# Performance work log

Hardware: AMD Instinct MI355X
Metric: run time of the kernel (lower is better)

The kernel has to match this reference:

```python
import jax, jax.numpy as jnp
import numpy as np

D_MODEL = 1024
D_STATE = 16
D_CONV = 4
EXPAND = 2
D_INNER = D_MODEL * EXPAND


def setup_inputs() -> dict:
    key = jax.random.key(0)
    ks = jax.random.split(key, 10)
    B, L = 2, 2048
    x = jax.random.normal(ks[0], (B, L, D_MODEL), jnp.float32)
    W_in = jax.random.normal(ks[1], (2 * D_INNER, D_MODEL), jnp.float32) * (1.0 / np.sqrt(D_MODEL))
    conv_w = jax.random.normal(ks[2], (D_INNER, 1, D_CONV), jnp.float32) * (1.0 / np.sqrt(D_CONV))
    conv_b = jax.random.normal(ks[3], (D_INNER,), jnp.float32) * 0.1
    W_x = jax.random.normal(ks[4], (2 * D_STATE + 1, D_INNER), jnp.float32) * (1.0 / np.sqrt(D_INNER))
    A_log = jnp.log(jnp.abs(jax.random.normal(ks[5], (D_INNER, D_STATE), jnp.float32)) + 1e-4)
    D_param = jnp.ones((D_INNER,), jnp.float32)
    W_dt = jax.random.normal(ks[6], (D_INNER, 1), jnp.float32)
    b_dt = jax.random.normal(ks[7], (D_INNER,), jnp.float32) * 0.1
    W_out = jax.random.normal(ks[8], (D_MODEL, D_INNER), jnp.float32) * (1.0 / np.sqrt(D_INNER))
    return {"x": x, "W_in": W_in, "conv_w": conv_w, "conv_b": conv_b, "W_x": W_x,
            "A_log": A_log, "D_param": D_param, "W_dt": W_dt, "b_dt": b_dt, "W_out": W_out}


def _forward(x, W_in, conv_w, conv_b, W_x, A_log, D_param, W_dt, b_dt, W_out):
    B, L, _ = x.shape
    xz = x @ W_in.T                                  # [B,L,2*d_inner]
    x_ssm, z = jnp.split(xz, 2, axis=-1)
    # causal depthwise conv: torch pads both sides d_conv-1 then truncates to L == left-pad only
    xc = jnp.transpose(x_ssm, (0, 2, 1))             # [B,d_inner,L]
    xc = jax.lax.conv_general_dilated(
        xc, conv_w, window_strides=(1,), padding=[(D_CONV - 1, 0)],
        feature_group_count=D_INNER, dimension_numbers=("NCH", "OIH", "NCH"))
    xc = xc + conv_b[None, :, None]
    x_ssm = jax.nn.silu(jnp.transpose(xc, (0, 2, 1)))  # [B,L,d_inner]
    proj = x_ssm @ W_x.T                              # [B,L,2*d_state+1]
    B_ssm = proj[..., :D_STATE]                       # [B,L,d_state]
    C_ssm = proj[..., D_STATE:2 * D_STATE]            # [B,L,d_state]
    dt = jax.nn.softplus(proj[..., -1:] * W_dt[:, 0] + b_dt)  # [B,L,d_inner]
    A = -jnp.exp(A_log)                               # [d_inner,d_state]

    def step(h, inp):
        dt_t, Bt, Ct, xt = inp                        # [B,d_inner],[B,n],[B,n],[B,d_inner]
        dA = jnp.exp(dt_t[..., None] * A)             # [B,d_inner,d_state]
        h = dA * h + (xt * dt_t)[..., None] * Bt[:, None, :]
        y = jnp.einsum("bdn,bn->bd", h, Ct)
        return h, y

    h0 = jnp.zeros((B, D_INNER, D_STATE), x.dtype)
    inputs = (jnp.transpose(dt, (1, 0, 2)), jnp.transpose(B_ssm, (1, 0, 2)),
              jnp.transpose(C_ssm, (1, 0, 2)), jnp.transpose(x_ssm, (1, 0, 2)))
    _, ys = jax.lax.scan(step, h0, inputs)            # ys: [L,B,d_inner]
    y = jnp.transpose(ys, (1, 0, 2)) + x_ssm * D_param
    y = y * jax.nn.silu(z)
    return y @ W_out.T


def reference(x, W_in, conv_w, conv_b, W_x, A_log, D_param, W_dt, b_dt, W_out):
    return _forward(x, W_in, conv_w, conv_b, W_x, A_log, D_param, W_dt, b_dt, W_out)
```

## Files before the change

### kernel.cpp

```cpp
#include <hip/hip_runtime.h>
#include <hip/hip_bf16.h>
#include <cstddef>

#define DMODEL 1024
#define DI     2048
#define DS     16
#define LSEQ   2048
#define BATCH  2
#define NC     128
#define TCH    (LSEQ / NC)

typedef __attribute__((ext_vector_type(8))) short short8;
typedef __attribute__((ext_vector_type(4))) float f32x4;
typedef __attribute__((ext_vector_type(2))) float f32x2;
typedef __attribute__((ext_vector_type(8))) unsigned short us8;

__device__ __forceinline__ unsigned short f2bf(float f) {
    unsigned int u = __float_as_uint(f);
    unsigned int r = (u + 0x7fff + ((u >> 16) & 1)) >> 16;
    return (unsigned short)r;
}
__device__ __forceinline__ float bf2f(unsigned short b) {
    return __uint_as_float(((unsigned int)b) << 16);
}

__device__ __forceinline__ float fexp2(float x) {
#if __has_builtin(__builtin_amdgcn_exp2f)
    return __builtin_amdgcn_exp2f(x);
#else
    return exp2f(x);
#endif
}
__device__ __forceinline__ float flog2(float x) {
#if __has_builtin(__builtin_amdgcn_logf)
    return __builtin_amdgcn_logf(x);
#else
    return log2f(x);
#endif
}

#define LOG2E 1.4426950408889634f
#define RLOG2E 0.6931471805599453f

__device__ __forceinline__ float softplus_f(float v) {
    return (v > 20.f) ? v : flog2(1.f + fexp2(v * LOG2E)) * RLOG2E;
}

__device__ __forceinline__ void gload_lds16(const void* g, void* l) {
    __builtin_amdgcn_global_load_lds(
        (const __attribute__((address_space(1))) unsigned int*)g,
        (__attribute__((address_space(3))) unsigned int*)l, 16, 0, 0);
}

__global__ void cvt_bf16(const float* __restrict__ in, unsigned short* __restrict__ out, int n8) {
    int i = blockIdx.x * 256 + threadIdx.x;
    if (i >= n8) return;
    const float4* p = reinterpret_cast<const float4*>(in) + i * 2;
    float4 v0 = p[0], v1 = p[1];
    us8 o;
    o[0] = f2bf(v0.x); o[1] = f2bf(v0.y); o[2] = f2bf(v0.z); o[3] = f2bf(v0.w);
    o[4] = f2bf(v1.x); o[5] = f2bf(v1.y); o[6] = f2bf(v1.z); o[7] = f2bf(v1.w);
    *reinterpret_cast<us8*>(out + (size_t)i * 8) = o;
}

__global__ void prep_wx(const float* __restrict__ wx, unsigned short* __restrict__ out) {
    int i = blockIdx.x * 256 + threadIdx.x;
    if (i >= 48 * 2048 / 8) return;
    size_t o = (size_t)i * 8;
    int row = (int)(o >> 11);
    us8 v;
    if (row < 33) {
        const float4* p = reinterpret_cast<const float4*>(wx + o);
        float4 v0 = p[0], v1 = p[1];
        v[0] = f2bf(v0.x); v[1] = f2bf(v0.y); v[2] = f2bf(v0.z); v[3] = f2bf(v0.w);
        v[4] = f2bf(v1.x); v[5] = f2bf(v1.y); v[6] = f2bf(v1.z); v[7] = f2bf(v1.w);
    } else {
        v = (us8)0;
    }
    *reinterpret_cast<us8*>(out + o) = v;
}

__global__ void prep_A(const float* __restrict__ A_log, float* __restrict__ At2) {
    int i = blockIdx.x * 256 + threadIdx.x;
    if (i >= DS * DI) return;
    int n = i / DI, d = i % DI;
    At2[i] = -__expf(A_log[d * DS + n]) * LOG2E;
}

#define NT1 32
__global__ __launch_bounds__(512, 1)
void gemm1_pipe(const unsigned short* __restrict__ A, const unsigned short* __restrict__ B,
                unsigned short* __restrict__ C) {
    __shared__ unsigned short lds[4][2][256 * 32];

    const int tid = threadIdx.x;
    const int wid = tid >> 6, ln = tid & 63;
    const int wm = wid >> 2, wn = wid & 3;

    int wg = blockIdx.x;
    wg = (wg & 7) * 32 + (wg >> 3);
    const int m0 = (wg >> 4) * 256;
    const int n0 = (wg & 15) * 256;

    const int srow = tid >> 2;
    const int sun  = tid & 3;
    const int ksrc = ((sun ^ ((srow >> 1) & 3)) * 8);

    const int fr = ln & 15;
    const int fku = (ln >> 4);

    f32x4 acc[8][4] = {};

    #define STAGE1(kt)                                                                     \
        do {                                                                               \
            const int bq_ = (kt) & 3;                                                      \
            gload_lds16(A + (size_t)(m0 + srow) * 1024 + (kt) * 32 + ksrc,                 \
                        &lds[bq_][0][srow * 32 + sun * 8]);                                \
            gload_lds16(A + (size_t)(m0 + 128 + srow) * 1024 + (kt) * 32 + ksrc,           \
                        &lds[bq_][0][(128 + srow) * 32 + sun * 8]);                        \
            gload_lds16(B + (size_t)(n0 + srow) * 1024 + (kt) * 32 + ksrc,                 \
                        &lds[bq_][1][srow * 32 + sun * 8]);                                \
            gload_lds16(B + (size_t)(n0 + 128 + srow) * 1024 + (kt) * 32 + ksrc,           \
                        &lds[bq_][1][(128 + srow) * 32 + sun * 8]);                        \
        } while (0)

    STAGE1(0); STAGE1(1); STAGE1(2);
    asm volatile("s_waitcnt vmcnt(8)" ::: "memory");
    __builtin_amdgcn_s_barrier();
    __builtin_amdgcn_sched_barrier(0);

    for (int kt = 0; kt < NT1; ++kt) {
        const int bq = kt & 3;
        if (kt + 3 < NT1) STAGE1(kt + 3);

        short8 af_lo[4], bfr[4], af_hi[4];
        #pragma unroll
        for (int i = 0; i < 4; ++i) {
            int r = wm * 128 + i * 16 + fr;
            int u = fku ^ ((r >> 1) & 3);
            af_lo[i] = *reinterpret_cast<const short8*>(&lds[bq][0][r * 32 + u * 8]);
        }
        #pragma unroll
        for (int j = 0; j < 4; ++j) {
            int r = wn * 64 + j * 16 + fr;
            int u = fku ^ ((r >> 1) & 3);
            bfr[j] = *reinterpret_cast<const short8*>(&lds[bq][1][r * 32 + u * 8]);
        }
        #pragma unroll
        for (int i = 0; i < 4; ++i) {
            int r = wm * 128 + (4 + i) * 16 + fr;
            int u = fku ^ ((r >> 1) & 3);
            af_hi[i] = *reinterpret_cast<const short8*>(&lds[bq][0][r * 32 + u * 8]);
        }
        __builtin_amdgcn_sched_barrier(0);
        __builtin_amdgcn_s_setprio(1);
        #pragma unroll
        for (int i = 0; i < 4; ++i)
            #pragma unroll
            for (int j = 0; j < 4; ++j)
                acc[i][j] = __builtin_amdgcn_mfma_f32_16x16x32_bf16(af_lo[i], bfr[j], acc[i][j], 0, 0, 0);
        __builtin_amdgcn_s_setprio(0);
        __builtin_amdgcn_sched_barrier(0);
        __builtin_amdgcn_s_setprio(1);
        #pragma unroll
        for (int i = 0; i < 4; ++i)
            #pragma unroll
            for (int j = 0; j < 4; ++j)
                acc[4 + i][j] = __builtin_amdgcn_mfma_f32_16x16x32_bf16(af_hi[i], bfr[j], acc[4 + i][j], 0, 0, 0);
        __builtin_amdgcn_s_setprio(0);
        __builtin_amdgcn_sched_barrier(0);

        if (kt < NT1 - 3)       asm volatile("s_waitcnt vmcnt(8)" ::: "memory");
        else if (kt == NT1 - 3) asm volatile("s_waitcnt vmcnt(4)" ::: "memory");
        else if (kt == NT1 - 2) asm volatile("s_waitcnt vmcnt(0)" ::: "memory");
        __builtin_amdgcn_s_barrier();
        __builtin_amdgcn_sched_barrier(0);
    }
    #undef STAGE1

    const int cr = (ln >> 4) * 4, cc = ln & 15;
    #pragma unroll
    for (int i = 0; i < 8; ++i) {
        int row = m0 + wm * 128 + i * 16 + cr;
        #pragma unroll
        for (int j = 0; j < 4; ++j) {
            int col = n0 + wn * 64 + j * 16 + cc;
            #pragma unroll
            for (int r = 0; r < 4; ++r)
                C[(size_t)(row + r) * 4096 + col] = f2bf(acc[i][j][r]);
        }
    }
}

#define NT3 64
__global__ __launch_bounds__(256, 2)
void gemm3_pipe(const unsigned short* __restrict__ A, int lda,
                const unsigned short* __restrict__ B,
                float* __restrict__ C) {
    __shared__ unsigned short As[4][128 * 32];
    __shared__ unsigned short Bs[4][64 * 32];

    const int tid = threadIdx.x;
    const int wid = tid >> 6, ln = tid & 63;
    const int wm = wid >> 1, wn = wid & 1;

    int wg = blockIdx.x;
    wg = (wg & 7) * 64 + (wg >> 3);
    const int m0 = (wg >> 4) * 128;
    const int n0 = (wg & 15) * 64;

    const int srow = tid >> 2;
    const int sun  = tid & 3;
    const int ksrc = ((sun ^ ((srow >> 1) & 3)) * 8);

    const int fr = ln & 15;
    const int fku = (ln >> 4);

    f32x4 acc[4][2] = {};

    #define STAGE3(kt)                                                                     \
        do {                                                                               \
            const int bq_ = (kt) & 3;                                                      \
            gload_lds16(A + (size_t)(m0 + srow) * lda + (kt) * 32 + ksrc,                  \
                        &As[bq_][srow * 32 + sun * 8]);                                    \
            gload_lds16(A + (size_t)(m0 + 64 + srow) * lda + (kt) * 32 + ksrc,             \
                        &As[bq_][(64 + srow) * 32 + sun * 8]);                             \
            gload_lds16(B + (size_t)(n0 + srow) * 2048 + (kt) * 32 + ksrc,                 \
                        &Bs[bq_][srow * 32 + sun * 8]);                                    \
        } while (0)

    STAGE3(0); STAGE3(1); STAGE3(2);
    asm volatile("s_waitcnt vmcnt(6)" ::: "memory");
    __builtin_amdgcn_s_barrier();
    __builtin_amdgcn_sched_barrier(0);

    for (int kt = 0; kt < NT3; ++kt) {
        const int bq = kt & 3;
        if (kt + 3 < NT3) STAGE3(kt + 3);

        short8 af[4], bfr[2];
        #pragma unroll
        for (int i = 0; i < 4; ++i) {
            int r = wm * 64 + i * 16 + fr;
            int u = fku ^ ((r >> 1) & 3);
            af[i] = *reinterpret_cast<const short8*>(&As[bq][r * 32 + u * 8]);
        }
        #pragma unroll
        for (int j = 0; j < 2; ++j) {
            int r = wn * 32 + j * 16 + fr;
            int u = fku ^ ((r >> 1) & 3);
            bfr[j] = *reinterpret_cast<const short8*>(&Bs[bq][r * 32 + u * 8]);
        }
        __builtin_amdgcn_sched_barrier(0);
        __builtin_amdgcn_s_setprio(1);
        #pragma unroll
        for (int i = 0; i < 4; ++i)
            #pragma unroll
            for (int j = 0; j < 2; ++j)
                acc[i][j] = __builtin_amdgcn_mfma_f32_16x16x32_bf16(af[i], bfr[j], acc[i][j], 0, 0, 0);
        __builtin_amdgcn_s_setprio(0);
        __builtin_amdgcn_sched_barrier(0);

        if (kt < NT3 - 3)       asm volatile("s_waitcnt vmcnt(6)" ::: "memory");
        else if (kt == NT3 - 3) asm volatile("s_waitcnt vmcnt(3)" ::: "memory");
        else if (kt == NT3 - 2) asm volatile("s_waitcnt vmcnt(0)" ::: "memory");
        __builtin_amdgcn_s_barrier();
        __builtin_amdgcn_sched_barrier(0);
    }
    #undef STAGE3

    const int cr = (ln >> 4) * 4, cc = ln & 15;
    #pragma unroll
    for (int i = 0; i < 4; ++i) {
        int row = m0 + wm * 64 + i * 16 + cr;
        #pragma unroll
        for (int j = 0; j < 2; ++j) {
            int col = n0 + wn * 32 + j * 16 + cc;
            #pragma unroll
            for (int r = 0; r < 4; ++r)
                C[(size_t)(row + r) * 1024 + col] = acc[i][j][r];
        }
    }
}

__global__ void conv_silu(const unsigned short* __restrict__ xzb, const float* __restrict__ cw,
                          const float* __restrict__ cb, unsigned short* __restrict__ xactb) {
    int i = blockIdx.x * 256 + threadIdx.x;
    if (i >= BATCH * LSEQ * DI / 8) return;
    int d0 = (i % (DI / 8)) * 8;
    int l  = (i / (DI / 8)) % LSEQ;
    int b  = i / ((DI / 8) * LSEQ);

    float4 w[8];
    #pragma unroll
    for (int j = 0; j < 8; ++j)
        w[j] = *reinterpret_cast<const float4*>(cw + (d0 + j) * 4);

    float acc[8];
    #pragma unroll
    for (int j = 0; j < 8; ++j) acc[j] = cb[d0 + j];

    #pragma unroll
    for (int t = 0; t < 4; ++t) {
        int ls = l - 3 + t;
        if (ls >= 0) {
            us8 v = *reinterpret_cast<const us8*>(xzb + (size_t)(b * LSEQ + ls) * 4096 + d0);
            #pragma unroll
            for (int j = 0; j < 8; ++j) {
                float wt = (t == 0) ? w[j].x : (t == 1) ? w[j].y : (t == 2) ? w[j].z : w[j].w;
                acc[j] += bf2f(v[j]) * wt;
            }
        }
    }
    us8 o;
    #pragma unroll
    for (int j = 0; j < 8; ++j) {
        float v = acc[j] / (1.f + __expf(-acc[j]));
        o[j] = f2bf(v);
    }
    *reinterpret_cast<us8*>(xactb + (size_t)i * 8) = o;
}

__global__ __launch_bounds__(256)
void gemm_proj_mfma(const unsigned short* __restrict__ Xb, const unsigned short* __restrict__ Wxb,
                    float* __restrict__ projp) {
    __shared__ unsigned short As[64 * 32];
    __shared__ unsigned short Bs[48 * 32];

    const int tid = threadIdx.x;
    const int wv = tid >> 6, ln = tid & 63;
    const int m0 = blockIdx.x * 64;
    const int kz = blockIdx.y;
    const int srow = tid >> 2, skoff = (tid & 3) * 8;
    const int fr = ln & 15, fk = (ln >> 4) * 8;

    f32x4 acc[3] = {};

    const int k0base = kz * 512;
    for (int k0 = k0base; k0 < k0base + 512; k0 += 32) {
        gload_lds16(Xb + (size_t)(m0 + srow) * DI + k0 + skoff, &As[wv * 512]);
        if (wv < 3)
            gload_lds16(Wxb + (size_t)srow * DI + k0 + skoff, &Bs[wv * 512]);
        __syncthreads();

        short8 af = *reinterpret_cast<const short8*>(&As[(wv * 16 + fr) * 32 + fk]);
        #pragma unroll
        for (int j = 0; j < 3; ++j) {
            short8 bf_ = *reinterpret_cast<const short8*>(&Bs[(j * 16 + fr) * 32 + fk]);
            acc[j] = __builtin_amdgcn_mfma_f32_16x16x32_bf16(af, bf_, acc[j], 0, 0, 0);
        }
        __syncthreads();
    }

    const int cr = (ln >> 4) * 4, cc = ln & 15;
    #pragma unroll
    for (int j = 0; j < 3; ++j) {
        int col = j * 16 + cc;
        if (col < 33) {
            #pragma unroll
            for (int r = 0; r < 4; ++r) {
                int row = m0 + wv * 16 + cr + r;
                projp[(size_t)row * 144 + kz * 36 + col] = acc[j][r];
            }
        }
    }
}

__global__ void proj_combine(const float* __restrict__ projp, float* __restrict__ proj) {
    int idx = blockIdx.x * 256 + threadIdx.x;
    if (idx >= BATCH * LSEQ * 33) return;
    int row = idx / 33, col = idx % 33;
    float s = 0.f;
    #pragma unroll
    for (int kz = 0; kz < 4; ++kz)
        s += projp[(size_t)row * 144 + kz * 36 + col];
    proj[(size_t)row * 36 + col] = s;
}

__global__ __launch_bounds__(256)
void scan_phase1(const unsigned short* __restrict__ xactb, const float* __restrict__ proj,
                 const float* __restrict__ At2, const float* __restrict__ W_dt,
                 const float* __restrict__ b_dt, unsigned short* __restrict__ Hend,
                 float* __restrict__ dtsum, unsigned short* __restrict__ yloc,
                 unsigned short* __restrict__ XZb) {
    const int d = blockIdx.x * 256 + threadIdx.x;
    const int c = blockIdx.y;
    const int b = blockIdx.z;

    f32x2 A2[DS / 2], h2[DS / 2];
    #pragma unroll
    for (int p = 0; p < DS / 2; ++p) {
        A2[p] = (f32x2){At2[(2 * p) * DI + d], At2[(2 * p + 1) * DI + d]};
        h2[p] = (f32x2){0.f, 0.f};
    }
    const float wdt = W_dt[d], bdt = b_dt[d];
    float ssum = 0.f;

    const int l0 = c * TCH;
    #pragma unroll 2
    for (int l = l0; l < l0 + TCH; ++l) {
        const size_t row = (size_t)(b * LSEQ + l);
        const float* pr = proj + row * 36;
        float dt = softplus_f(pr[32] * wdt + bdt);
        ssum += dt;
        XZb[row * 4096 + d] = f2bf(ssum);
        float x = bf2f(xactb[row * DI + d]);
        float xdt = x * dt;
        f32x2 xdt2 = (f32x2){xdt, xdt};
        f32x2 y2 = (f32x2){0.f, 0.f};
        #pragma unroll
        for (int p = 0; p < DS / 2; ++p) {
            f32x2 t = A2[p] * dt;
            f32x2 e2 = (f32x2){fexp2(t.x), fexp2(t.y)};
            h2[p] = e2 * h2[p] + xdt2 * (f32x2){pr[2 * p], pr[2 * p + 1]};
            y2 += h2[p] * (f32x2){pr[16 + 2 * p], pr[17 + 2 * p]};
        }
        yloc[row * DI + d] = f2bf(y2.x + y2.y);
    }
    size_t base = ((size_t)(b * NC + c) * DS) * DI + d;
    #pragma unroll
    for (int p = 0; p < DS / 2; ++p) {
        Hend[base + (size_t)(2 * p) * DI]     = f2bf(h2[p].x);
        Hend[base + (size_t)(2 * p + 1) * DI] = f2bf(h2[p].y);
    }
    dtsum[(size_t)(b * NC + c) * DI + d] = ssum;
}

__global__ void scan_phase2(unsigned short* __restrict__ H, const float* __restrict__ dtsum,
                            const float* __restrict__ At2) {
    int idx = blockIdx.x * 256 + threadIdx.x;
    int b = idx / (DS * DI);
    int r = idx % (DS * DI);
    int n = r / DI, d = r % DI;
    float A2 = At2[n * DI + d];
    float h = 0.f;
    #pragma unroll 4
    for (int c = 0; c < NC; ++c) {
        size_t off = ((size_t)(b * NC + c) * DS + n) * DI + d;
        float He = bf2f(H[off]);
        float P = fexp2(A2 * dtsum[(size_t)(b * NC + c) * DI + d]);
        H[off] = f2bf(h);
        h = P * h + He;
    }
}

__global__ __launch_bounds__(256)
void scan_phase3(const unsigned short* __restrict__ xactb, const unsigned short* __restrict__ yloc,
                 const float* __restrict__ proj, const float* __restrict__ At2,
                 const float* __restrict__ Dp, const unsigned short* __restrict__ Hin,
                 unsigned short* __restrict__ XZb) {
    const int tid = threadIdx.x;
    const int d = blockIdx.x * 256 + tid;
    const int c = blockIdx.y;
    const int b = blockIdx.z;

    f32x2 A2[DS / 2], Hn2[DS / 2];
    size_t hbase = ((size_t)(b * NC + c) * DS) * DI + d;
    #pragma unroll
    for (int p = 0; p < DS / 2; ++p) {
        A2[p]  = (f32x2){At2[(2 * p) * DI + d], At2[(2 * p + 1) * DI + d]};
        Hn2[p] = (f32x2){bf2f(Hin[hbase + (size_t)(2 * p) * DI]),
                         bf2f(Hin[hbase + (size_t)(2 * p + 1) * DI])};
    }

    const float Dv = Dp[d];
    const int l0 = c * TCH;
    #pragma unroll 2
    for (int l = l0; l < l0 + TCH; ++l) {
        const size_t row = (size_t)(b * LSEQ + l);
        const float* pr = proj + row * 36;
        unsigned short* xzrow = XZb + row * 4096;
        float S  = bf2f(xzrow[d]);
        float yl = bf2f(yloc[row * DI + d]);
        float x  = bf2f(xactb[row * DI + d]);
        float z  = bf2f(xzrow[2048 + d]);
        f32x2 corr2 = (f32x2){0.f, 0.f};
        #pragma unroll
        for (int p = 0; p < DS / 2; ++p) {
            f32x2 t = A2[p] * S;
            f32x2 e2 = (f32x2){fexp2(t.x), fexp2(t.y)};
            corr2 += (f32x2){pr[16 + 2 * p], pr[17 + 2 * p]} * e2 * Hn2[p];
        }
        float y = yl + corr2.x + corr2.y + x * Dv;
        float sz = z / (1.f + __expf(-z));
        xzrow[d] = f2bf(y * sz);
    }
}

extern "C" void kernel_launch(void* const* d_in, const int* in_sizes, int n_in,
                              void* d_out, int out_size, void* d_ws, size_t ws_size,
                              hipStream_t stream) {
    const float* x      = (const float*)d_in[0];
    const float* W_in   = (const float*)d_in[1];
    const float* conv_w = (const float*)d_in[2];
    const float* conv_b = (const float*)d_in[3];
    const float* W_x    = (const float*)d_in[4];
    const float* A_log  = (const float*)d_in[5];
    const float* Dp     = (const float*)d_in[6];
    const float* W_dt   = (const float*)d_in[7];
    const float* b_dt   = (const float*)d_in[8];
    const float* W_out  = (const float*)d_in[9];
    float* out = (float*)d_out;

    char* ws = (char*)d_ws;
    unsigned short* XZb   = (unsigned short*)(ws + 0);
    unsigned short* XACTB = (unsigned short*)(ws + 33554432);
    unsigned short* Xb    = (unsigned short*)(ws + 50331648);
    unsigned short* W_inb = (unsigned short*)(ws + 58720256);
    unsigned short* Hbuf  = (unsigned short*)(ws + 67108864);
    unsigned short* YLOC  = (unsigned short*)(ws + 83886080);
    float* PROJ  = (float*)(ws + 100663296);
    float* DTSUM = (float*)(ws + 101711872);
    float* PROJP = (float*)(ws + 103809024);
    float* Abuf  = (float*)(ws + 106954752);
    unsigned short* W_outb = (unsigned short*)(ws + 108003328);
    unsigned short* Wxb48  = (unsigned short*)(ws + 112197632);

    const int M = BATCH * LSEQ;

    cvt_bf16<<<M * DMODEL / 8 / 256, 256, 0, stream>>>(x, Xb, M * DMODEL / 8);
    cvt_bf16<<<2 * DI * DMODEL / 8 / 256, 256, 0, stream>>>(W_in, W_inb, 2 * DI * DMODEL / 8);
    prep_wx<<<48, 256, 0, stream>>>(W_x, Wxb48);
    prep_A<<<DS * DI / 256, 256, 0, stream>>>(A_log, Abuf);

    gemm1_pipe<<<256, 512, 0, stream>>>(Xb, W_inb, XZb);

    conv_silu<<<BATCH * LSEQ * DI / 8 / 256, 256, 0, stream>>>(XZb, conv_w, conv_b, XACTB);

    gemm_proj_mfma<<<dim3(M / 64, 4), 256, 0, stream>>>(XACTB, Wxb48, PROJP);
    proj_combine<<<(M * 33 + 255) / 256, 256, 0, stream>>>(PROJP, PROJ);

    scan_phase1<<<dim3(DI / 256, NC, BATCH), 256, 0, stream>>>(
        XACTB, PROJ, Abuf, W_dt, b_dt, Hbuf, DTSUM, YLOC, XZb);
    scan_phase2<<<BATCH * DS * DI / 256, 256, 0, stream>>>(Hbuf, DTSUM, Abuf);
    scan_phase3<<<dim3(DI / 256, NC, BATCH), 256, 0, stream>>>(
        XACTB, YLOC, PROJ, Abuf, Dp, Hbuf, XZb);

    cvt_bf16<<<DMODEL * DI / 8 / 256, 256, 0, stream>>>(W_out, W_outb, DMODEL * DI / 8);
    gemm3_pipe<<<512, 256, 0, stream>>>(XZb, 4096, W_outb, out);
}
```

Measured before the change: 211.5 us.

## Restructure input GEMM into 8-phase double-buffered pipeline with K=64 tiles

Rewrites the input projection GEMM to use K=64 tiles in two LDS buffers instead of four K=32 buffers. Each K-tile is split into four sub-phases, and global-to-LDS loads for future tiles are interleaved with the MFMA groups. The swizzle changes to 8 slots per row. The aim is to hide load latency better and cut barrier overhead per unit of math, at the cost of more barriers per tile and more complex vmcnt accounting.

```diff
diff --git a/kernel.cpp b/kernel.cpp
--- a/kernel.cpp
+++ b/kernel.cpp
@@ -87,11 +87,12 @@
     At2[i] = -__expf(A_log[d * DS + n]) * LOG2E;
 }
 
-#define NT1 32
+#define T1 16
 __global__ __launch_bounds__(512, 1)
-void gemm1_pipe(const unsigned short* __restrict__ A, const unsigned short* __restrict__ B,
-                unsigned short* __restrict__ C) {
-    __shared__ unsigned short lds[4][2][256 * 32];
+void gemm1_8ph(const unsigned short* __restrict__ A, const unsigned short* __restrict__ B,
+               unsigned short* __restrict__ C) {
+    __shared__ unsigned short ldsA[2][256 * 64];
+    __shared__ unsigned short ldsB[2][256 * 64];
 
     const int tid = threadIdx.x;
     const int wid = tid >> 6, ln = tid & 63;
@@ -102,86 +103,100 @@
     const int m0 = (wg >> 4) * 256;
     const int n0 = (wg & 15) * 256;
 
-    const int srow = tid >> 2;
-    const int sun  = tid & 3;
-    const int ksrc = ((sun ^ ((srow >> 1) & 3)) * 8);
+    const int rr = tid >> 3;
+    const int s  = tid & 7;
+    const int sgk = (s ^ (rr & 7)) * 8;
 
     const int fr = ln & 15;
     const int fku = (ln >> 4);
 
     f32x4 acc[8][4] = {};
 
-    #define STAGE1(kt)                                                                     \
-        do {                                                                               \
-            const int bq_ = (kt) & 3;                                                      \
-            gload_lds16(A + (size_t)(m0 + srow) * 1024 + (kt) * 32 + ksrc,                 \
-                        &lds[bq_][0][srow * 32 + sun * 8]);                                \
-            gload_lds16(A + (size_t)(m0 + 128 + srow) * 1024 + (kt) * 32 + ksrc,           \
-                        &lds[bq_][0][(128 + srow) * 32 + sun * 8]);                        \
-            gload_lds16(B + (size_t)(n0 + srow) * 1024 + (kt) * 32 + ksrc,                 \
-                        &lds[bq_][1][srow * 32 + sun * 8]);                                \
-            gload_lds16(B + (size_t)(n0 + 128 + srow) * 1024 + (kt) * 32 + ksrc,           \
-                        &lds[bq_][1][(128 + srow) * 32 + sun * 8]);                        \
+    #define STAGE_A(buf, t, p)                                                           \
+        do {                                                                             \
+            int row_ = (p) * 32 + (rr & 31) + (rr >> 5) * 128;                           \
+            gload_lds16(A + (size_t)(m0 + row_) * 1024 + (t) * 64 + sgk,                 \
+                        &ldsA[buf][row_ * 64 + s * 8]);                                  \
         } while (0)
-
-    STAGE1(0); STAGE1(1); STAGE1(2);
-    asm volatile("s_waitcnt vmcnt(8)" ::: "memory");
+    #define STAGE_B(buf, t, p)                                                           \
+        do {                                                                             \
+            int row_ = (p) * 64 + rr;                                                    \
+            gload_lds16(B + (size_t)(n0 + row_) * 1024 + (t) * 64 + sgk,                 \
+                        &ldsB[buf][row_ * 64 + s * 8]);                                  \
+        } while (0)
+
+    #pragma unroll
+    for (int p = 0; p < 4; ++p) { STAGE_A(0, 0, p); STAGE_B(0, 0, p); }
+    #pragma unroll
+    for (int p = 0; p < 3; ++p) { STAGE_A(1, 1, p); STAGE_B(1, 1, p); }
+    asm volatile("s_waitcnt vmcnt(6)" ::: "memory");
     __builtin_amdgcn_s_barrier();
     __builtin_amdgcn_sched_barrier(0);
 
-    for (int kt = 0; kt < NT1; ++kt) {
-        const int bq = kt & 3;
-        if (kt + 3 < NT1) STAGE1(kt + 3);
-
-        short8 af_lo[4], bfr[4], af_hi[4];
-        #pragma unroll
-        for (int i = 0; i < 4; ++i) {
-            int r = wm * 128 + i * 16 + fr;
-            int u = fku ^ ((r >> 1) & 3);
-            af_lo[i] = *reinterpret_cast<const short8*>(&lds[bq][0][r * 32 + u * 8]);
-        }
-        #pragma unroll
-        for (int j = 0; j < 4; ++j) {
-            int r = wn * 64 + j * 16 + fr;
-            int u = fku ^ ((r >> 1) & 3);
-            bfr[j] = *reinterpret_cast<const short8*>(&lds[bq][1][r * 32 + u * 8]);
-        }
-        #pragma unroll
-        for (int i = 0; i < 4; ++i) {
-            int r = wm * 128 + (4 + i) * 16 + fr;
-            int u = fku ^ ((r >> 1) & 3);
-            af_hi[i] = *reinterpret_cast<const short8*>(&lds[bq][0][r * 32 + u * 8]);
-        }
-        __builtin_amdgcn_sched_barrier(0);
-        __builtin_amdgcn_s_setprio(1);
-        #pragma unroll
-        for (int i = 0; i < 4; ++i)
-            #pragma unroll
-            for (int j = 0; j < 4; ++j)
-                acc[i][j] = __builtin_amdgcn_mfma_f32_16x16x32_bf16(af_lo[i], bfr[j], acc[i][j], 0, 0, 0);
-        __builtin_amdgcn_s_setprio(0);
-        __builtin_amdgcn_sched_barrier(0);
-        __builtin_amdgcn_s_setprio(1);
-        #pragma unroll
-        for (int i = 0; i < 4; ++i)
-            #pragma unroll
-            for (int j = 0; j < 4; ++j)
-                acc[4 + i][j] = __builtin_amdgcn_mfma_f32_16x16x32_bf16(af_hi[i], bfr[j], acc[4 + i][j], 0, 0, 0);
-        __builtin_amdgcn_s_setprio(0);
-        __builtin_amdgcn_sched_barrier(0);
-
-        if (kt < NT1 - 3)       asm volatile("s_waitcnt vmcnt(8)" ::: "memory");
-        else if (kt == NT1 - 3) asm volatile("s_waitcnt vmcnt(4)" ::: "memory");
-        else if (kt == NT1 - 2) asm volatile("s_waitcnt vmcnt(0)" ::: "memory");
-        __builtin_amdgcn_s_barrier();
-        __builtin_amdgcn_sched_barrier(0);
-    }
-    #undef STAGE1
+    #pragma unroll 2
+    for (int t = 0; t < T1; ++t) {
+        const int c = t & 1;
+        short8 bfr[4][2];
+
+        #pragma unroll
+        for (int q = 0; q < 4; ++q) {
+            short8 afr[2][2];
+            #pragma unroll
+            for (int m = 0; m < 2; ++m)
+                #pragma unroll
+                for (int kk = 0; kk < 2; ++kk) {
+                    int row = wm * 128 + q * 32 + m * 16 + fr;
+                    int slot = (kk * 4 + fku) ^ (row & 7);
+                    afr[m][kk] = *reinterpret_cast<const short8*>(&ldsA[c][row * 64 + slot * 8]);
+                }
+            if (q == 0) {
+                #pragma unroll
+                for (int n = 0; n < 4; ++n)
+                    #pragma unroll
+                    for (int kk = 0; kk < 2; ++kk) {
+                        int row = wn * 64 + n * 16 + fr;
+                        int slot = (kk * 4 + fku) ^ (row & 7);
+                        bfr[n][kk] = *reinterpret_cast<const short8*>(&ldsB[c][row * 64 + slot * 8]);
+                    }
+            }
+            if (q == 0) {
+                if (t + 1 < T1) { STAGE_A(c ^ 1, t + 1, 3); STAGE_B(c ^ 1, t + 1, 3); }
+            } else {
+                if (t + 2 < T1) { STAGE_A(c, t + 2, q - 1); STAGE_B(c, t + 2, q - 1); }
+            }
+
+            __builtin_amdgcn_s_barrier();
+            asm volatile("s_waitcnt lgkmcnt(0)" ::: "memory");
+            __builtin_amdgcn_sched_barrier(0);
+
+            __builtin_amdgcn_s_setprio(1);
+            #pragma unroll
+            for (int m = 0; m < 2; ++m)
+                #pragma unroll
+                for (int n = 0; n < 4; ++n) {
+                    acc[q * 2 + m][n] = __builtin_amdgcn_mfma_f32_16x16x32_bf16(
+                        afr[m][0], bfr[n][0], acc[q * 2 + m][n], 0, 0, 0);
+                    acc[q * 2 + m][n] = __builtin_amdgcn_mfma_f32_16x16x32_bf16(
+                        afr[m][1], bfr[n][1], acc[q * 2 + m][n], 0, 0, 0);
+                }
+            __builtin_amdgcn_s_setprio(0);
+            __builtin_amdgcn_sched_barrier(0);
+
+            if (q == 3) {
+                if (t < T1 - 2) asm volatile("s_waitcnt vmcnt(6)" ::: "memory");
+                else            asm volatile("s_waitcnt vmcnt(0)" ::: "memory");
+            }
+            __builtin_amdgcn_s_barrier();
+            __builtin_amdgcn_sched_barrier(0);
+        }
+    }
+    #undef STAGE_A
+    #undef STAGE_B
 
     const int cr = (ln >> 4) * 4, cc = ln & 15;
     #pragma unroll
     for (int i = 0; i < 8; ++i) {
-        int row = m0 + wm * 128 + i * 16 + cr;
+        int row = m0 + wm * 128 + (i >> 1) * 32 + (i & 1) * 16 + cr;
         #pragma unroll
         for (int j = 0; j < 4; ++j) {
             int col = n0 + wn * 64 + j * 16 + cc;
@@ -523,7 +538,7 @@
     prep_wx<<<48, 256, 0, stream>>>(W_x, Wxb48);
     prep_A<<<DS * DI / 256, 256, 0, stream>>>(A_log, Abuf);
 
-    gemm1_pipe<<<256, 512, 0, stream>>>(Xb, W_inb, XZb);
+    gemm1_8ph<<<256, 512, 0, stream>>>(Xb, W_inb, XZb);
 
     conv_silu<<<BATCH * LSEQ * DI / 8 / 256, 256, 0, stream>>>(XZb, conv_w, conv_b, XACTB);
 
```

Result: no change. 212.6 us (+0.5%).
